# Kernel optimization log

Measured on AMD Instinct MI355X. Metric: run time of the kernel, lower is better.

The kernel has to match this reference:

```python
import jax, jax.numpy as jnp
import numpy as np

# Matcher weights (Deformable-DETR defaults used by SimPLR-style repos)
COST_CLASS, COST_BBOX, COST_GIOU = 2.0, 5.0, 2.0
ALPHA, GAMMA = 0.25, 2.0  # focal cost hyperparams
EPS = 1e-8


def box_cxcywh_to_xyxy(b):
    cx, cy, w, h = jnp.split(b, 4, axis=-1)
    return jnp.concatenate([cx - 0.5 * w, cy - 0.5 * h, cx + 0.5 * w, cy + 0.5 * h], axis=-1)


def generalized_box_iou(b1, b2):
    # b1 [Q,4], b2 [T,4] in xyxy -> [Q,T]
    area1 = (b1[:, 2] - b1[:, 0]) * (b1[:, 3] - b1[:, 1])
    area2 = (b2[:, 2] - b2[:, 0]) * (b2[:, 3] - b2[:, 1])
    lt = jnp.maximum(b1[:, None, :2], b2[None, :, :2])
    rb = jnp.minimum(b1[:, None, 2:], b2[None, :, 2:])
    wh = jnp.clip(rb - lt, 0.0)
    inter = wh[..., 0] * wh[..., 1]
    union = area1[:, None] + area2[None, :] - inter
    iou = inter / union
    lt2 = jnp.minimum(b1[:, None, :2], b2[None, :, :2])
    rb2 = jnp.maximum(b1[:, None, 2:], b2[None, :, 2:])
    wh2 = jnp.clip(rb2 - lt2, 0.0)
    hull = wh2[..., 0] * wh2[..., 1]
    return iou - (hull - union) / hull


def cost_matrix(logits, boxes, tgt_ids, tgt_boxes):
    # per-image: logits [Q,C], boxes [Q,4] cxcywh, tgt_ids [T], tgt_boxes [T,4]
    prob = jax.nn.sigmoid(logits)
    neg = (1.0 - ALPHA) * (prob ** GAMMA) * (-jnp.log(1.0 - prob + EPS))
    pos = ALPHA * ((1.0 - prob) ** GAMMA) * (-jnp.log(prob + EPS))
    cost_class = pos[:, tgt_ids] - neg[:, tgt_ids]                    # [Q,T]
    cost_bbox = jnp.abs(boxes[:, None, :] - tgt_boxes[None, :, :]).sum(-1)  # L1 cdist [Q,T]
    cost_giou = -generalized_box_iou(box_cxcywh_to_xyxy(boxes), box_cxcywh_to_xyxy(tgt_boxes))
    return COST_BBOX * cost_bbox + COST_CLASS * cost_class + COST_GIOU * cost_giou


def lsa(cost):
    # Hungarian (Jonker-Volgenant / e-maxx shortest augmenting path), minimizes.
    # cost [n, m] with n <= m; returns col4row: column assigned to each row.
    n, m = cost.shape
    u = np.zeros(n + 1)
    v = np.zeros(m + 1)
    p = np.zeros(m + 1, dtype=np.int64)   # p[j] = row matched to col j (1-based), 0 = free
    way = np.zeros(m + 1, dtype=np.int64)
    for i in range(1, n + 1):
        p[0] = i
        j0 = 0
        minv = np.full(m + 1, np.inf)
        used = np.zeros(m + 1, dtype=bool)
        while True:
            used[j0] = True
            i0 = p[j0]
            free = ~used
            free[0] = False
            cur = cost[i0 - 1] - u[i0] - v[1:]
            better = np.zeros(m + 1, dtype=bool)
            better[1:] = free[1:] & (cur < minv[1:])
            minv[better] = cur[better[1:]]
            way[better] = j0
            cand = np.where(free[1:], minv[1:], np.inf)
            j1 = int(np.argmin(cand)) + 1
            delta = cand[j1 - 1]
            u[p[used]] += delta
            v[used] -= delta
            minv[free] -= delta
            j0 = j1
            if p[j0] == 0:
                break
        while j0 != 0:
            j1 = way[j0]
            p[j0] = p[j1]
            j0 = j1
    col4row = np.zeros(n, dtype=np.int64)
    for j in range(1, m + 1):
        if p[j] > 0:
            col4row[p[j] - 1] = j - 1
    return col4row


_batched_cost = jax.jit(jax.vmap(cost_matrix, in_axes=(0, 0, 0, 0)))


def setup_inputs() -> dict:
    key = jax.random.key(0)
    k1, k2, k3, k4 = jax.random.split(key, 4)
    bs, nq, nc, nt = 32, 900, 1203, 100
    return {
        "pred_logits": jax.random.normal(k1, (bs, nq, nc), dtype=jnp.float32),
        "pred_boxes": jax.random.uniform(k2, (bs, nq, 4), dtype=jnp.float32),
        "tgt_labels": jax.random.randint(k3, (bs, nt), 0, nc, dtype=jnp.int64),
        "tgt_boxes": jax.random.uniform(k4, (bs, nt, 4), dtype=jnp.float32),
    }


def reference(pred_logits, pred_boxes, tgt_labels, tgt_boxes):
    # Cost blocks [bs, Q, T] (identical to the per-image diagonal blocks of the
    # torch code's [bs, Q, sum_T] view, which are the only parts used).
    C = _batched_cost(pred_logits, pred_boxes, tgt_labels, tgt_boxes)
    Cn = np.asarray(jax.device_get(C))
    rows, cols = [], []
    for b in range(Cn.shape[0]):
        col4row = lsa(Cn[b].T)          # [T]: matched query index per target
        order = np.argsort(col4row)     # scipy returns row indices sorted ascending
        rows.append(col4row[order])     # index_i: selected prediction indices
        cols.append(order)              # index_j: corresponding target indices
    pred_idx = jnp.asarray(np.stack(rows), dtype=jnp.int64)  # [bs, T]
    tgt_idx = jnp.asarray(np.stack(cols), dtype=jnp.int64)   # [bs, T]
    return C, pred_idx, tgt_idx
```

## Files before the change

kernel.cpp:

```cpp
#include <hip/hip_runtime.h>
#include <math.h>

#define BS 32
#define NQ 900
#define NC 1203
#define NT 100
#define SLOTS 15
#define K8 8

__device__ float g_CT[(size_t)BS * NT * NQ];
__device__ unsigned long long g_topk[(size_t)BS * NT * K8];

__device__ __forceinline__ unsigned long long packf(float f, int col) {
    unsigned k = __float_as_uint(f);
    k = (k & 0x80000000u) ? ~k : (k | 0x80000000u);
    return ((unsigned long long)k << 32) | (unsigned)col;
}
__device__ __forceinline__ float unpack_val(unsigned long long p) {
    unsigned k = (unsigned)(p >> 32);
    unsigned bits = (k & 0x80000000u) ? (k ^ 0x80000000u) : ~k;
    return __uint_as_float(bits);
}
__device__ __forceinline__ int unpack_col(unsigned long long p) {
    return (int)(p & 0xFFFFFFFFu);
}

__global__ __launch_bounds__(128) void cost_kernel(
    const float* __restrict__ logits, const float* __restrict__ boxes,
    const int* __restrict__ tlabels, const float* __restrict__ tboxes,
    float* __restrict__ C)
{
    int bq = blockIdx.x;
    int b = bq / NQ, q = bq % NQ;
    int t = threadIdx.x;

    const float* pb = boxes + (size_t)(b * NQ + q) * 4;
    float pcx = pb[0], pcy = pb[1], pw = pb[2], ph = pb[3];

    if (t < NT) {
        int id = tlabels[b * NT + t];
        float x = logits[(size_t)(b * NQ + q) * NC + id];
        float prob = 1.0f / (1.0f + expf(-x));
        float neg = 0.75f * (prob * prob) * (-logf(1.0f - prob + 1e-8f));
        float pos = 0.25f * ((1.0f - prob) * (1.0f - prob)) * (-logf(prob + 1e-8f));
        float cclass = pos - neg;

        const float* tb = tboxes + (size_t)(b * NT + t) * 4;
        float tcx = tb[0], tcy = tb[1], tw = tb[2], th = tb[3];
        float cbbox = fabsf(pcx - tcx) + fabsf(pcy - tcy) + fabsf(pw - tw) + fabsf(ph - th);

        float p0 = pcx - 0.5f * pw, p1 = pcy - 0.5f * ph;
        float p2 = pcx + 0.5f * pw, p3 = pcy + 0.5f * ph;
        float t0 = tcx - 0.5f * tw, t1 = tcy - 0.5f * th;
        float t2 = tcx + 0.5f * tw, t3 = tcy + 0.5f * th;
        float area1 = (p2 - p0) * (p3 - p1);
        float area2 = (t2 - t0) * (t3 - t1);
        float ltx = fmaxf(p0, t0), lty = fmaxf(p1, t1);
        float rbx = fminf(p2, t2), rby = fminf(p3, t3);
        float wx = fmaxf(rbx - ltx, 0.0f), wy = fmaxf(rby - lty, 0.0f);
        float inter = wx * wy;
        float uni = area1 + area2 - inter;
        float iou = inter / uni;
        float l2x = fminf(p0, t0), l2y = fminf(p1, t1);
        float r2x = fmaxf(p2, t2), r2y = fmaxf(p3, t3);
        float hx = fmaxf(r2x - l2x, 0.0f), hy = fmaxf(r2y - l2y, 0.0f);
        float hull = hx * hy;
        float giou = iou - (hull - uni) / hull;

        C[(size_t)(b * NQ + q) * NT + t] =
            5.0f * cbbox + 2.0f * cclass + 2.0f * (-giou);
    }
}

__global__ __launch_bounds__(256) void transpose_kernel(const float* __restrict__ C)
{
    __shared__ float tile[64][101];
    int b = blockIdx.x / 15;
    int chunk = blockIdx.x % 15;
    int q0 = chunk * 64;
    int nq = (q0 + 64 <= NQ) ? 64 : (NQ - q0);
    int tid = threadIdx.x;

    const float* Cb = C + (size_t)b * NQ * NT;
    for (int e = tid; e < nq * NT; e += 256) {
        int qq = e / NT, t = e % NT;
        tile[qq][t] = Cb[(size_t)(q0 + qq) * NT + t];
    }
    __syncthreads();
    float* CTb = g_CT + (size_t)b * NT * NQ;
    for (int e = tid; e < NT * nq; e += 256) {
        int t = e / nq, qq = e % nq;
        CTb[(size_t)t * NQ + q0 + qq] = tile[qq][t];
    }
}

__global__ __launch_bounds__(64) void topk_kernel()
{
    int bi = blockIdx.x;
    const float* row = g_CT + (size_t)bi * NQ;
    int lane = threadIdx.x;

    unsigned long long r[K8];
    #pragma unroll
    for (int m = 0; m < K8; ++m) r[m] = 0xFFFFFFFFFFFFFFFFull;

    #pragma unroll
    for (int k = 0; k < SLOTS; ++k) {
        int j = (k << 6) + lane;
        if ((k < SLOTS - 1) || (j < NQ)) {
            unsigned long long key = packf(row[j], j);
            #pragma unroll
            for (int m = 0; m < K8; ++m) {
                unsigned long long lo = key < r[m] ? key : r[m];
                unsigned long long hi = key < r[m] ? r[m] : key;
                r[m] = lo; key = hi;
            }
        }
    }
    #pragma unroll
    for (int off = 32; off; off >>= 1) {
        unsigned long long bv[K8], t[K8];
        #pragma unroll
        for (int m = 0; m < K8; ++m) bv[m] = __shfl_down(r[m], off);
        #pragma unroll
        for (int m = 0; m < K8; ++m) {
            unsigned long long x = bv[K8 - 1 - m];
            t[m] = r[m] < x ? r[m] : x;
        }
        #pragma unroll
        for (int d = 4; d; d >>= 1) {
            #pragma unroll
            for (int m = 0; m < K8; ++m) {
                if (!(m & d)) {
                    unsigned long long a = t[m], b2 = t[m | d];
                    t[m] = a < b2 ? a : b2;
                    t[m | d] = a < b2 ? b2 : a;
                }
            }
        }
        #pragma unroll
        for (int m = 0; m < K8; ++m) r[m] = t[m];
    }
    if (lane == 0) {
        #pragma unroll
        for (int m = 0; m < K8; ++m) g_topk[(size_t)bi * K8 + m] = r[m];
    }
}

__global__ __launch_bounds__(64) void jv_kernel(
    float* __restrict__ pred_out, float* __restrict__ tgt_out)
{
    int b = blockIdx.x;
    const float* CTb = g_CT + (size_t)b * NT * NQ;
    int lane = threadIdx.x;
    const double INF = __builtin_huge_val();

    __shared__ double u[NT];
    __shared__ double vsh[NQ];
    __shared__ double distA[128];
    __shared__ int pathA[128];
    __shared__ int asgCols[128];
    __shared__ int pos4col[NQ];
    __shared__ int row4col[NQ];
    __shared__ int col4row[NT];
    __shared__ int aminsh[NT];
    __shared__ int freeRows[NT + 4];
    __shared__ int parked[NT];
    __shared__ int srList[140];
    __shared__ unsigned long long tksh[NT][K8];
    __shared__ unsigned char visits[NT];
    __shared__ int nFreeSh, nParkSh, asgCountSh;

    for (int j = lane; j < NQ; j += 64) { vsh[j] = 0.0; row4col[j] = 0x7fffffff; pos4col[j] = -1; }
    {
        const unsigned long long* src = g_topk + (size_t)b * NT * K8;
        for (int e = lane; e < NT * K8; e += 64) ((unsigned long long*)tksh)[e] = src[e];
    }
    for (int i = lane; i < NT; i += 64) { col4row[i] = -1; visits[i] = 0; }
    if (lane == 0) { nFreeSh = 0; nParkSh = 0; asgCountSh = 0; }
    __syncthreads();
    for (int i = lane; i < NT; i += 64) {
        unsigned long long tk = tksh[i][0];
        aminsh[i] = unpack_col(tk);
        u[i] = (double)unpack_val(tk);
    }
    __syncthreads();

    for (int i = lane; i < NT; i += 64) atomicMin(&row4col[aminsh[i]], i);
    __syncthreads();
    if (lane == 0) {
        int n = 0, cnt = 0;
        for (int i = 0; i < NT; ++i) {
            int j = aminsh[i];
            if (row4col[j] == i) { col4row[i] = j; pos4col[j] = cnt; asgCols[cnt++] = j; }
            else freeRows[n++] = i;
        }
        nFreeSh = n; asgCountSh = cnt;
    }
    __syncthreads();
    for (int j = lane; j < NQ; j += 64)
        if (row4col[j] == 0x7fffffff) row4col[j] = -1;
    __syncthreads();

    int guard = 0;
    while (guard++ < 300) {
        int nf = nFreeSh;
        if (nf == 0) break;
        int i = freeRows[nf - 1];
        if (visits[i] >= 2) {
            if (lane == 0) { nFreeSh = nf - 1; parked[nParkSh] = i; nParkSh++; }
            __syncthreads();
            continue;
        }
        if (lane == 0) visits[i]++;
        int asgCount = asgCountSh;
        const float* rowp = CTb + (size_t)i * NQ;

        double m1 = INF, m2 = INF; int j1 = -1;
        bool haveFree = (lane < K8) && (row4col[unpack_col(tksh[i][lane])] < 0);
        unsigned long long bal = __ballot(haveFree);
        if (__popcll(bal) >= 2) {
            #pragma unroll
            for (int s = 0; s < 2; ++s) {
                int pos = lane + (s << 6);
                if (pos < asgCount) {
                    int j = asgCols[pos];
                    double cur = (double)rowp[j] - vsh[j];
                    if (cur < m1) { m2 = m1; m1 = cur; j1 = j; }
                    else if (cur < m2) m2 = cur;
                }
            }
            if (haveFree) {
                unsigned long long tk = tksh[i][lane];
                double cur = (double)unpack_val(tk);
                int j = unpack_col(tk);
                if (cur < m1) { m2 = m1; m1 = cur; j1 = j; }
                else if (cur < m2) m2 = cur;
            }
        } else {
            #pragma unroll
            for (int k = 0; k < SLOTS; ++k) {
                int j = (k << 6) + lane;
                if ((k < SLOTS - 1) || (j < NQ)) {
                    double cur = (double)rowp[j] - vsh[j];
                    if (cur < m1) { m2 = m1; m1 = cur; j1 = j; }
                    else if (cur < m2) m2 = cur;
                }
            }
        }
        for (int off = 32; off; off >>= 1) {
            double o1 = __shfl_down(m1, off); int oj = __shfl_down(j1, off);
            double o2 = __shfl_down(m2, off);
            if (o1 < m1 || (o1 == m1 && (unsigned)oj < (unsigned)j1)) { m2 = fmin(m1, o2); m1 = o1; j1 = oj; }
            else m2 = fmin(m2, o1);
        }
        if (lane == 0) {
            u[i] = m2;
            vsh[j1] -= (m2 - m1);
            int inc = row4col[j1];
            row4col[j1] = i; col4row[i] = j1;
            int n = nf - 1;
            if (inc >= 0) { col4row[inc] = -1; freeRows[n++] = inc; }
            else { pos4col[j1] = asgCountSh; asgCols[asgCountSh] = j1; asgCountSh++; }
            nFreeSh = n;
        }
        __syncthreads();
    }
    if (lane == 0) {
        while (nFreeSh > 0) { nFreeSh--; parked[nParkSh] = freeRows[nFreeSh]; nParkSh++; }
    }
    __syncthreads();

    int np = nParkSh;
    for (int f = 0; f < np; ++f) {
        int curRow = parked[f];
        int asgCount = asgCountSh;
        double mvA = INF, mvB = INF;
        bool pA = false, pB = false;
        for (int pos = lane; pos < asgCount; pos += 64) distA[pos] = INF;
        double bestFree = INF; int bfCol = -1, bfRow = -1;
        double minVal = 0.0; int i = curRow; int nSr = 1;
        if (lane == 0) srList[0] = curRow;
        __syncthreads();

        int g2 = 0; bool sink = false;
        while (!sink && g2++ < 120) {
            const float* rowp = CTb + (size_t)i * NQ;
            double ui = u[i];
            {
                int pos = lane;
                if (pos < asgCount && !pA) {
                    int j = asgCols[pos];
                    double cur = minVal + (double)rowp[j] - ui - vsh[j];
                    if (cur < mvA) { mvA = cur; distA[pos] = cur; pathA[pos] = i; }
                }
                pos = lane + 64;
                if (pos < asgCount && !pB) {
                    int j = asgCols[pos];
                    double cur = minVal + (double)rowp[j] - ui - vsh[j];
                    if (cur < mvB) { mvB = cur; distA[pos] = cur; pathA[pos] = i; }
                }
            }
            double fc = INF; int fj = -1;
            if (lane < K8) {
                unsigned long long tk = tksh[i][lane];
                int j = unpack_col(tk);
                if (row4col[j] < 0) { fc = minVal + (double)unpack_val(tk) - ui; fj = j; }
            }
            if (__ballot(fc < INF) == 0ull) {
                #pragma unroll
                for (int k = 0; k < SLOTS; ++k) {
                    int j = (k << 6) + lane;
                    if (((k < SLOTS - 1) || (j < NQ)) && row4col[j] < 0) {
                        double cur = minVal + (double)rowp[j] - ui;
                        if (cur < fc) { fc = cur; fj = j; }
                    }
                }
            }
            double pv; int ppos;
            double pva = pA ? INF : mvA, pvb = pB ? INF : mvB;
            if (pvb < pva) { pv = pvb; ppos = lane + 64; } else { pv = pva; ppos = lane; }
            for (int off = 32; off; off >>= 1) {
                double o = __shfl_down(pv, off); int op = __shfl_down(ppos, off);
                if (o < pv || (o == pv && op < ppos)) { pv = o; ppos = op; }
                double of = __shfl_down(fc, off); int ofj = __shfl_down(fj, off);
                if (of < fc || (of == fc && (unsigned)ofj < (unsigned)fj)) { fc = of; fj = ofj; }
            }
            pv = __shfl(pv, 0); ppos = __shfl(ppos, 0);
            fc = __shfl(fc, 0); fj = __shfl(fj, 0);
            if (fc < bestFree) { bestFree = fc; bfCol = fj; bfRow = i; }
            if (bestFree <= pv) { minVal = bestFree; sink = true; }
            else {
                minVal = pv;
                if (lane == (ppos & 63)) { if (ppos < 64) pA = true; else pB = true; }
                i = row4col[asgCols[ppos]];
                if (lane == 0) srList[nSr] = i;
                nSr++;
            }
        }
        __syncthreads();

        if (lane == 0) {
            u[curRow] += minVal;
            for (int t2 = 1; t2 < nSr; ++t2) {
                int ri = srList[t2];
                u[ri] += minVal - distA[pos4col[col4row[ri]]];
            }
        }
        {
            int pos = lane;
            if (pos < asgCount && pA) vsh[asgCols[pos]] -= minVal - distA[pos];
            pos = lane + 64;
            if (pos < asgCount && pB) vsh[asgCols[pos]] -= minVal - distA[pos];
        }
        if (lane == 0) {
            int j = bfCol, ri = bfRow; int g3 = 0;
            while (g3++ < 128) {
                row4col[j] = ri;
                int tj = col4row[ri]; col4row[ri] = j;
                if (ri == curRow) break;
                j = tj; ri = pathA[pos4col[j]];
            }
            pos4col[bfCol] = asgCountSh; asgCols[asgCountSh] = bfCol; asgCountSh++;
        }
        __syncthreads();
    }

    for (int i2 = lane; i2 < NT; i2 += 64) {
        int ci = col4row[i2];
        int rank = 0;
        for (int k2 = 0; k2 < NT; ++k2) rank += (col4row[k2] < ci);
        pred_out[b * NT + rank] = (float)ci;
        tgt_out[b * NT + rank] = (float)i2;
    }
}

extern "C" void kernel_launch(void* const* d_in, const int* in_sizes, int n_in,
                              void* d_out, int out_size, void* d_ws, size_t ws_size,
                              hipStream_t stream) {
    const float* logits = (const float*)d_in[0];
    const float* boxes  = (const float*)d_in[1];
    const int*   tlab   = (const int*)d_in[2];
    const float* tboxes = (const float*)d_in[3];

    float* out  = (float*)d_out;
    float* C    = out;
    float* pred = out + (size_t)BS * NQ * NT;
    float* tgt  = pred + BS * NT;

    cost_kernel<<<BS * NQ, 128, 0, stream>>>(logits, boxes, tlab, tboxes, C);
    transpose_kernel<<<BS * 15, 256, 0, stream>>>(C);
    topk_kernel<<<BS * NT, 64, 0, stream>>>();
    jv_kernel<<<BS, 64, 0, stream>>>(pred, tgt);
}
```

Before: 109.0 us.

## Fuse transpose and top-k selection into one kernel over target-row chunks

Merges the transpose kernel and the per-row top-k kernel into a single kernel. Each block loads 8 target columns for all queries into shared memory, writes the transposed rows to the global buffer, and runs the top-8 selection directly from shared memory, one wavefront per row. This removes a kernel launch and the re-read of the transposed matrix from global memory. In exchange there are far fewer blocks (416), and the strided loads of 8 floats per query row may coalesce poorly.

```diff
diff --git a/kernel.cpp b/kernel.cpp
--- a/kernel.cpp
+++ b/kernel.cpp
@@ -7,6 +7,8 @@
 #define NT 100
 #define SLOTS 15
 #define K8 8
+#define TCH 8
+#define NCHUNK 13
 
 __device__ float g_CT[(size_t)BS * NT * NQ];
 __device__ unsigned long long g_topk[(size_t)BS * NT * K8];
@@ -72,78 +74,78 @@
     }
 }
 
-__global__ __launch_bounds__(256) void transpose_kernel(const float* __restrict__ C)
+__global__ __launch_bounds__(256) void ttopk_kernel(const float* __restrict__ C)
 {
-    __shared__ float tile[64][101];
-    int b = blockIdx.x / 15;
-    int chunk = blockIdx.x % 15;
-    int q0 = chunk * 64;
-    int nq = (q0 + 64 <= NQ) ? 64 : (NQ - q0);
+    __shared__ float tile[TCH][NQ];
+    int blk = blockIdx.x;
+    int b = blk / NCHUNK, chunk = blk % NCHUNK;
+    int t0 = chunk * TCH;
+    int nrows = (t0 + TCH <= NT) ? TCH : (NT - t0);
     int tid = threadIdx.x;
+    int w = tid >> 6, lane = tid & 63;
 
     const float* Cb = C + (size_t)b * NQ * NT;
-    for (int e = tid; e < nq * NT; e += 256) {
-        int qq = e / NT, t = e % NT;
-        tile[qq][t] = Cb[(size_t)(q0 + qq) * NT + t];
-    }
-    __syncthreads();
+    for (int e = tid; e < NQ * TCH; e += 256) {
+        int q = e >> 3, tt = e & 7;
+        if (tt < nrows) tile[tt][q] = Cb[(size_t)q * NT + t0 + tt];
+    }
+    __syncthreads();
+
     float* CTb = g_CT + (size_t)b * NT * NQ;
-    for (int e = tid; e < NT * nq; e += 256) {
-        int t = e / nq, qq = e % nq;
-        CTb[(size_t)t * NQ + q0 + qq] = tile[qq][t];
-    }
-}
-
-__global__ __launch_bounds__(64) void topk_kernel()
-{
-    int bi = blockIdx.x;
-    const float* row = g_CT + (size_t)bi * NQ;
-    int lane = threadIdx.x;
-
-    unsigned long long r[K8];
-    #pragma unroll
-    for (int m = 0; m < K8; ++m) r[m] = 0xFFFFFFFFFFFFFFFFull;
-
-    #pragma unroll
-    for (int k = 0; k < SLOTS; ++k) {
-        int j = (k << 6) + lane;
-        if ((k < SLOTS - 1) || (j < NQ)) {
-            unsigned long long key = packf(row[j], j);
+    for (int tt = 0; tt < nrows; ++tt)
+        for (int q = tid; q < NQ; q += 256)
+            CTb[(size_t)(t0 + tt) * NQ + q] = tile[tt][q];
+
+    for (int pass = 0; pass < 2; ++pass) {
+        int tt = w + pass * 4;
+        if (tt >= nrows) continue;
+
+        unsigned long long r[K8];
+        #pragma unroll
+        for (int m = 0; m < K8; ++m) r[m] = 0xFFFFFFFFFFFFFFFFull;
+
+        #pragma unroll
+        for (int k = 0; k < SLOTS; ++k) {
+            int j = (k << 6) + lane;
+            if ((k < SLOTS - 1) || (j < NQ)) {
+                unsigned long long key = packf(tile[tt][j], j);
+                #pragma unroll
+                for (int m = 0; m < K8; ++m) {
+                    unsigned long long lo = key < r[m] ? key : r[m];
+                    unsigned long long hi = key < r[m] ? r[m] : key;
+                    r[m] = lo; key = hi;
+                }
+            }
+        }
+        #pragma unroll
+        for (int off = 32; off; off >>= 1) {
+            unsigned long long bv[K8], tmp[K8];
+            #pragma unroll
+            for (int m = 0; m < K8; ++m) bv[m] = __shfl_down(r[m], off);
             #pragma unroll
             for (int m = 0; m < K8; ++m) {
-                unsigned long long lo = key < r[m] ? key : r[m];
-                unsigned long long hi = key < r[m] ? r[m] : key;
-                r[m] = lo; key = hi;
-            }
-        }
-    }
-    #pragma unroll
-    for (int off = 32; off; off >>= 1) {
-        unsigned long long bv[K8], t[K8];
-        #pragma unroll
-        for (int m = 0; m < K8; ++m) bv[m] = __shfl_down(r[m], off);
-        #pragma unroll
-        for (int m = 0; m < K8; ++m) {
-            unsigned long long x = bv[K8 - 1 - m];
-            t[m] = r[m] < x ? r[m] : x;
-        }
-        #pragma unroll
-        for (int d = 4; d; d >>= 1) {
-            #pragma unroll
-            for (int m = 0; m < K8; ++m) {
-                if (!(m & d)) {
-                    unsigned long long a = t[m], b2 = t[m | d];
-                    t[m] = a < b2 ? a : b2;
-                    t[m | d] = a < b2 ? b2 : a;
-                }
-            }
-        }
-        #pragma unroll
-        for (int m = 0; m < K8; ++m) r[m] = t[m];
-    }
-    if (lane == 0) {
-        #pragma unroll
-        for (int m = 0; m < K8; ++m) g_topk[(size_t)bi * K8 + m] = r[m];
+                unsigned long long x = bv[K8 - 1 - m];
+                tmp[m] = r[m] < x ? r[m] : x;
+            }
+            #pragma unroll
+            for (int d = 4; d; d >>= 1) {
+                #pragma unroll
+                for (int m = 0; m < K8; ++m) {
+                    if (!(m & d)) {
+                        unsigned long long a = tmp[m], b2 = tmp[m | d];
+                        tmp[m] = a < b2 ? a : b2;
+                        tmp[m | d] = a < b2 ? b2 : a;
+                    }
+                }
+            }
+            #pragma unroll
+            for (int m = 0; m < K8; ++m) r[m] = tmp[m];
+        }
+        if (lane == 0) {
+            #pragma unroll
+            for (int m = 0; m < K8; ++m)
+                g_topk[(size_t)(b * NT + t0 + tt) * K8 + m] = r[m];
+        }
     }
 }
 
@@ -389,7 +391,6 @@
     float* tgt  = pred + BS * NT;
 
     cost_kernel<<<BS * NQ, 128, 0, stream>>>(logits, boxes, tlab, tboxes, C);
-    transpose_kernel<<<BS * 15, 256, 0, stream>>>(C);
-    topk_kernel<<<BS * NT, 64, 0, stream>>>();
+    ttopk_kernel<<<BS * NCHUNK, 256, 0, stream>>>(C);
     jv_kernel<<<BS, 64, 0, stream>>>(pred, tgt);
 }
```

Measured after the change: 128.8 us. 18.1% more time.

## Run JV auction phase with four wavefronts bidding on free rows concurrently

Applied to the files above, without the earlier changes.

The JV kernel grows from one wavefront to four. In the auction phase each wavefront computes the bid for a different free row, and thread 0 then applies the bids serially, requeueing any row whose bid clashes with an earlier one. The kernel also reads the untransposed C output with a strided access of stride NT instead of the transposed g_CT rows, which makes the row scans uncoalesced. The augmenting-path phase still runs on wave 0 alone, with extra shared-memory handoffs and barriers. The change may also alter the auction's visit order and so the final assignment.

```diff
diff --git a/kernel.cpp b/kernel.cpp
--- a/kernel.cpp
+++ b/kernel.cpp
@@ -7,6 +7,8 @@
 #define NT 100
 #define SLOTS 15
 #define K8 8
+#define JBLK 256
+#define NW 4
 
 __device__ float g_CT[(size_t)BS * NT * NQ];
 __device__ unsigned long long g_topk[(size_t)BS * NT * K8];
@@ -119,27 +121,27 @@
     }
     #pragma unroll
     for (int off = 32; off; off >>= 1) {
-        unsigned long long bv[K8], t[K8];
+        unsigned long long bv[K8], tmp[K8];
         #pragma unroll
         for (int m = 0; m < K8; ++m) bv[m] = __shfl_down(r[m], off);
         #pragma unroll
         for (int m = 0; m < K8; ++m) {
             unsigned long long x = bv[K8 - 1 - m];
-            t[m] = r[m] < x ? r[m] : x;
+            tmp[m] = r[m] < x ? r[m] : x;
         }
         #pragma unroll
         for (int d = 4; d; d >>= 1) {
             #pragma unroll
             for (int m = 0; m < K8; ++m) {
                 if (!(m & d)) {
-                    unsigned long long a = t[m], b2 = t[m | d];
-                    t[m] = a < b2 ? a : b2;
-                    t[m | d] = a < b2 ? b2 : a;
+                    unsigned long long a = tmp[m], b2 = tmp[m | d];
+                    tmp[m] = a < b2 ? a : b2;
+                    tmp[m | d] = a < b2 ? b2 : a;
                 }
             }
         }
         #pragma unroll
-        for (int m = 0; m < K8; ++m) r[m] = t[m];
+        for (int m = 0; m < K8; ++m) r[m] = tmp[m];
     }
     if (lane == 0) {
         #pragma unroll
@@ -147,12 +149,14 @@
     }
 }
 
-__global__ __launch_bounds__(64) void jv_kernel(
+__global__ __launch_bounds__(JBLK) void jv_kernel(
+    const float* __restrict__ C,
     float* __restrict__ pred_out, float* __restrict__ tgt_out)
 {
     int b = blockIdx.x;
-    const float* CTb = g_CT + (size_t)b * NT * NQ;
-    int lane = threadIdx.x;
+    const float* Cb = C + (size_t)b * NQ * NT;
+    int tid = threadIdx.x;
+    int w = tid >> 6, lane = tid & 63;
     const double INF = __builtin_huge_val();
 
     __shared__ double u[NT];
@@ -164,31 +168,33 @@
     __shared__ int row4col[NQ];
     __shared__ int col4row[NT];
     __shared__ int aminsh[NT];
-    __shared__ int freeRows[NT + 4];
+    __shared__ int freeRows[NT + 8];
     __shared__ int parked[NT];
     __shared__ int srList[140];
     __shared__ unsigned long long tksh[NT][K8];
     __shared__ unsigned char visits[NT];
+    __shared__ double pm1[NW], pm2[NW];
+    __shared__ int pj1[NW], prow[NW];
     __shared__ int nFreeSh, nParkSh, asgCountSh;
 
-    for (int j = lane; j < NQ; j += 64) { vsh[j] = 0.0; row4col[j] = 0x7fffffff; pos4col[j] = -1; }
+    for (int j = tid; j < NQ; j += JBLK) { vsh[j] = 0.0; row4col[j] = 0x7fffffff; pos4col[j] = -1; }
     {
         const unsigned long long* src = g_topk + (size_t)b * NT * K8;
-        for (int e = lane; e < NT * K8; e += 64) ((unsigned long long*)tksh)[e] = src[e];
-    }
-    for (int i = lane; i < NT; i += 64) { col4row[i] = -1; visits[i] = 0; }
-    if (lane == 0) { nFreeSh = 0; nParkSh = 0; asgCountSh = 0; }
-    __syncthreads();
-    for (int i = lane; i < NT; i += 64) {
+        for (int e = tid; e < NT * K8; e += JBLK) ((unsigned long long*)tksh)[e] = src[e];
+    }
+    for (int i = tid; i < NT; i += JBLK) { col4row[i] = -1; visits[i] = 0; }
+    if (tid == 0) { nFreeSh = 0; nParkSh = 0; asgCountSh = 0; }
+    __syncthreads();
+    for (int i = tid; i < NT; i += JBLK) {
         unsigned long long tk = tksh[i][0];
         aminsh[i] = unpack_col(tk);
         u[i] = (double)unpack_val(tk);
     }
     __syncthreads();
 
-    for (int i = lane; i < NT; i += 64) atomicMin(&row4col[aminsh[i]], i);
-    __syncthreads();
-    if (lane == 0) {
+    for (int i = tid; i < NT; i += JBLK) atomicMin(&row4col[aminsh[i]], i);
+    __syncthreads();
+    if (tid == 0) {
         int n = 0, cnt = 0;
         for (int i = 0; i < NT; ++i) {
             int j = aminsh[i];
@@ -198,75 +204,85 @@
         nFreeSh = n; asgCountSh = cnt;
     }
     __syncthreads();
-    for (int j = lane; j < NQ; j += 64)
+    for (int j = tid; j < NQ; j += JBLK)
         if (row4col[j] == 0x7fffffff) row4col[j] = -1;
     __syncthreads();
 
     int guard = 0;
-    while (guard++ < 300) {
+    while (guard++ < 250) {
         int nf = nFreeSh;
         if (nf == 0) break;
-        int i = freeRows[nf - 1];
-        if (visits[i] >= 2) {
-            if (lane == 0) { nFreeSh = nf - 1; parked[nParkSh] = i; nParkSh++; }
-            __syncthreads();
-            continue;
-        }
-        if (lane == 0) visits[i]++;
-        int asgCount = asgCountSh;
-        const float* rowp = CTb + (size_t)i * NQ;
-
-        double m1 = INF, m2 = INF; int j1 = -1;
-        bool haveFree = (lane < K8) && (row4col[unpack_col(tksh[i][lane])] < 0);
-        unsigned long long bal = __ballot(haveFree);
-        if (__popcll(bal) >= 2) {
-            #pragma unroll
-            for (int s = 0; s < 2; ++s) {
-                int pos = lane + (s << 6);
-                if (pos < asgCount) {
-                    int j = asgCols[pos];
-                    double cur = (double)rowp[j] - vsh[j];
+        int take = nf < NW ? nf : NW;
+        if (w < take) {
+            int i = freeRows[nf - 1 - w];
+            int asgCount = asgCountSh;
+
+            double m1 = INF, m2 = INF; int j1 = -1;
+            bool haveFree = (lane < K8) && (row4col[unpack_col(tksh[i][lane])] < 0);
+            unsigned long long bal = __ballot(haveFree);
+            if (__popcll(bal) >= 2) {
+                #pragma unroll
+                for (int s = 0; s < 2; ++s) {
+                    int pos = lane + (s << 6);
+                    if (pos < asgCount) {
+                        int j = asgCols[pos];
+                        double cur = (double)Cb[(size_t)j * NT + i] - vsh[j];
+                        if (cur < m1) { m2 = m1; m1 = cur; j1 = j; }
+                        else if (cur < m2) m2 = cur;
+                    }
+                }
+                if (haveFree) {
+                    unsigned long long tk = tksh[i][lane];
+                    double cur = (double)unpack_val(tk);
+                    int j = unpack_col(tk);
                     if (cur < m1) { m2 = m1; m1 = cur; j1 = j; }
                     else if (cur < m2) m2 = cur;
                 }
-            }
-            if (haveFree) {
-                unsigned long long tk = tksh[i][lane];
-                double cur = (double)unpack_val(tk);
-                int j = unpack_col(tk);
-                if (cur < m1) { m2 = m1; m1 = cur; j1 = j; }
-                else if (cur < m2) m2 = cur;
-            }
-        } else {
-            #pragma unroll
-            for (int k = 0; k < SLOTS; ++k) {
-                int j = (k << 6) + lane;
-                if ((k < SLOTS - 1) || (j < NQ)) {
-                    double cur = (double)rowp[j] - vsh[j];
-                    if (cur < m1) { m2 = m1; m1 = cur; j1 = j; }
-                    else if (cur < m2) m2 = cur;
-                }
-            }
-        }
-        for (int off = 32; off; off >>= 1) {
-            double o1 = __shfl_down(m1, off); int oj = __shfl_down(j1, off);
-            double o2 = __shfl_down(m2, off);
-            if (o1 < m1 || (o1 == m1 && (unsigned)oj < (unsigned)j1)) { m2 = fmin(m1, o2); m1 = o1; j1 = oj; }
-            else m2 = fmin(m2, o1);
-        }
-        if (lane == 0) {
-            u[i] = m2;
-            vsh[j1] -= (m2 - m1);
-            int inc = row4col[j1];
-            row4col[j1] = i; col4row[i] = j1;
-            int n = nf - 1;
-            if (inc >= 0) { col4row[inc] = -1; freeRows[n++] = inc; }
-            else { pos4col[j1] = asgCountSh; asgCols[asgCountSh] = j1; asgCountSh++; }
+            } else {
+                #pragma unroll
+                for (int k = 0; k < SLOTS; ++k) {
+                    int j = (k << 6) + lane;
+                    if ((k < SLOTS - 1) || (j < NQ)) {
+                        double cur = (double)Cb[(size_t)j * NT + i] - vsh[j];
+                        if (cur < m1) { m2 = m1; m1 = cur; j1 = j; }
+                        else if (cur < m2) m2 = cur;
+                    }
+                }
+            }
+            for (int off = 32; off; off >>= 1) {
+                double o1 = __shfl_down(m1, off); int oj = __shfl_down(j1, off);
+                double o2 = __shfl_down(m2, off);
+                if (o1 < m1 || (o1 == m1 && (unsigned)oj < (unsigned)j1)) { m2 = fmin(m1, o2); m1 = o1; j1 = oj; }
+                else m2 = fmin(m2, o1);
+            }
+            if (lane == 0) { pm1[w] = m1; pm2[w] = m2; pj1[w] = j1; prow[w] = i; }
+        }
+        __syncthreads();
+        if (tid == 0) {
+            int n = nf - take;
+            int cj[NW]; int nc = 0;
+            for (int k = 0; k < take; ++k) {
+                int i = prow[k];
+                if (visits[i] >= 2) { parked[nParkSh] = i; nParkSh++; continue; }
+                int j1 = pj1[k];
+                bool clash = false;
+                for (int k2 = 0; k2 < nc; ++k2) if (cj[k2] == j1) clash = true;
+                if (clash) { freeRows[n++] = i; continue; }
+                cj[nc++] = j1;
+                visits[i]++;
+                double m1 = pm1[k], m2 = pm2[k];
+                u[i] = m2;
+                vsh[j1] -= (m2 - m1);
+                int inc = row4col[j1];
+                row4col[j1] = i; col4row[i] = j1;
+                if (inc >= 0) { col4row[inc] = -1; freeRows[n++] = inc; }
+                else { pos4col[j1] = asgCountSh; asgCols[asgCountSh] = j1; asgCountSh++; }
+            }
             nFreeSh = n;
         }
         __syncthreads();
     }
-    if (lane == 0) {
+    if (tid == 0) {
         while (nFreeSh > 0) { nFreeSh--; parked[nParkSh] = freeRows[nFreeSh]; nParkSh++; }
     }
     __syncthreads();
@@ -277,96 +293,102 @@
         int asgCount = asgCountSh;
         double mvA = INF, mvB = INF;
         bool pA = false, pB = false;
-        for (int pos = lane; pos < asgCount; pos += 64) distA[pos] = INF;
         double bestFree = INF; int bfCol = -1, bfRow = -1;
         double minVal = 0.0; int i = curRow; int nSr = 1;
-        if (lane == 0) srList[0] = curRow;
+        if (w == 0) {
+            for (int pos = lane; pos < asgCount; pos += 64) distA[pos] = INF;
+            if (lane == 0) srList[0] = curRow;
+        }
         __syncthreads();
 
-        int g2 = 0; bool sink = false;
-        while (!sink && g2++ < 120) {
-            const float* rowp = CTb + (size_t)i * NQ;
-            double ui = u[i];
-            {
-                int pos = lane;
-                if (pos < asgCount && !pA) {
-                    int j = asgCols[pos];
-                    double cur = minVal + (double)rowp[j] - ui - vsh[j];
-                    if (cur < mvA) { mvA = cur; distA[pos] = cur; pathA[pos] = i; }
-                }
-                pos = lane + 64;
-                if (pos < asgCount && !pB) {
-                    int j = asgCols[pos];
-                    double cur = minVal + (double)rowp[j] - ui - vsh[j];
-                    if (cur < mvB) { mvB = cur; distA[pos] = cur; pathA[pos] = i; }
-                }
-            }
-            double fc = INF; int fj = -1;
-            if (lane < K8) {
-                unsigned long long tk = tksh[i][lane];
-                int j = unpack_col(tk);
-                if (row4col[j] < 0) { fc = minVal + (double)unpack_val(tk) - ui; fj = j; }
-            }
-            if (__ballot(fc < INF) == 0ull) {
-                #pragma unroll
-                for (int k = 0; k < SLOTS; ++k) {
-                    int j = (k << 6) + lane;
-                    if (((k < SLOTS - 1) || (j < NQ)) && row4col[j] < 0) {
-                        double cur = minVal + (double)rowp[j] - ui;
-                        if (cur < fc) { fc = cur; fj = j; }
+        if (w == 0) {
+            int g2 = 0; bool sink = false;
+            while (!sink && g2++ < 120) {
+                double ui = u[i];
+                {
+                    int pos = lane;
+                    if (pos < asgCount && !pA) {
+                        int j = asgCols[pos];
+                        double cur = minVal + (double)Cb[(size_t)j * NT + i] - ui - vsh[j];
+                        if (cur < mvA) { mvA = cur; distA[pos] = cur; pathA[pos] = i; }
                     }
-                }
-            }
-            double pv; int ppos;
-            double pva = pA ? INF : mvA, pvb = pB ? INF : mvB;
-            if (pvb < pva) { pv = pvb; ppos = lane + 64; } else { pv = pva; ppos = lane; }
-            for (int off = 32; off; off >>= 1) {
-                double o = __shfl_down(pv, off); int op = __shfl_down(ppos, off);
-                if (o < pv || (o == pv && op < ppos)) { pv = o; ppos = op; }
-                double of = __shfl_down(fc, off); int ofj = __shfl_down(fj, off);
-                if (of < fc || (of == fc && (unsigned)ofj < (unsigned)fj)) { fc = of; fj = ofj; }
-            }
-            pv = __shfl(pv, 0); ppos = __shfl(ppos, 0);
-            fc = __shfl(fc, 0); fj = __shfl(fj, 0);
-            if (fc < bestFree) { bestFree = fc; bfCol = fj; bfRow = i; }
-            if (bestFree <= pv) { minVal = bestFree; sink = true; }
-            else {
-                minVal = pv;
-                if (lane == (ppos & 63)) { if (ppos < 64) pA = true; else pB = true; }
-                i = row4col[asgCols[ppos]];
-                if (lane == 0) srList[nSr] = i;
-                nSr++;
-            }
+                    pos = lane + 64;
+                    if (pos < asgCount && !pB) {
+                        int j = asgCols[pos];
+                        double cur = minVal + (double)Cb[(size_t)j * NT + i] - ui - vsh[j];
+                        if (cur < mvB) { mvB = cur; distA[pos] = cur; pathA[pos] = i; }
+                    }
+                }
+                double fc = INF; int fj = -1;
+                if (lane < K8) {
+                    unsigned long long tk = tksh[i][lane];
+                    int j = unpack_col(tk);
+                    if (row4col[j] < 0) { fc = minVal + (double)unpack_val(tk) - ui; fj = j; }
+                }
+                if (__ballot(fc < INF) == 0ull) {
+                    #pragma unroll
+                    for (int k = 0; k < SLOTS; ++k) {
+                        int j = (k << 6) + lane;
+                        if (((k < SLOTS - 1) || (j < NQ)) && row4col[j] < 0) {
+                            double cur = minVal + (double)Cb[(size_t)j * NT + i] - ui;
+                            if (cur < fc) { fc = cur; fj = j; }
+                        }
+                    }
+                }
+                double pv; int ppos;
+                double pva = pA ? INF : mvA, pvb = pB ? INF : mvB;
+                if (pvb < pva) { pv = pvb; ppos = lane + 64; } else { pv = pva; ppos = lane; }
+                for (int off = 32; off; off >>= 1) {
+                    double o = __shfl_down(pv, off); int op = __shfl_down(ppos, off);
+                    if (o < pv || (o == pv && op < ppos)) { pv = o; ppos = op; }
+                    double of = __shfl_down(fc, off); int ofj = __shfl_down(fj, off);
+                    if (of < fc || (of == fc && (unsigned)ofj < (unsigned)fj)) { fc = of; fj = ofj; }
+                }
+                pv = __shfl(pv, 0); ppos = __shfl(ppos, 0);
+                fc = __shfl(fc, 0); fj = __shfl(fj, 0);
+                if (fc < bestFree) { bestFree = fc; bfCol = fj; bfRow = i; }
+                if (bestFree <= pv) { minVal = bestFree; sink = true; }
+                else {
+                    minVal = pv;
+                    if (lane == (ppos & 63)) { if (ppos < 64) pA = true; else pB = true; }
+                    i = row4col[asgCols[ppos]];
+                    if (lane == 0) srList[nSr] = i;
+                    nSr++;
+                }
+            }
+            if (lane == 0) { pm1[0] = minVal; pj1[0] = bfCol; prow[0] = bfRow; pm2[0] = (double)nSr; }
         }
         __syncthreads();
 
-        if (lane == 0) {
-            u[curRow] += minVal;
-            for (int t2 = 1; t2 < nSr; ++t2) {
+        if (tid == 0) {
+            double mv = pm1[0]; int ns = (int)pm2[0];
+            u[curRow] += mv;
+            for (int t2 = 1; t2 < ns; ++t2) {
                 int ri = srList[t2];
-                u[ri] += minVal - distA[pos4col[col4row[ri]]];
-            }
-        }
-        {
+                u[ri] += mv - distA[pos4col[col4row[ri]]];
+            }
+        }
+        if (w == 0) {
+            double mv = pm1[0];
             int pos = lane;
-            if (pos < asgCount && pA) vsh[asgCols[pos]] -= minVal - distA[pos];
+            if (pos < asgCount && pA) vsh[asgCols[pos]] -= mv - distA[pos];
             pos = lane + 64;
-            if (pos < asgCount && pB) vsh[asgCols[pos]] -= minVal - distA[pos];
-        }
-        if (lane == 0) {
-            int j = bfCol, ri = bfRow; int g3 = 0;
+            if (pos < asgCount && pB) vsh[asgCols[pos]] -= mv - distA[pos];
+        }
+        if (tid == 0) {
+            int j = pj1[0], ri = prow[0]; int g3 = 0;
             while (g3++ < 128) {
                 row4col[j] = ri;
                 int tj = col4row[ri]; col4row[ri] = j;
                 if (ri == curRow) break;
                 j = tj; ri = pathA[pos4col[j]];
             }
-            pos4col[bfCol] = asgCountSh; asgCols[asgCountSh] = bfCol; asgCountSh++;
+            pos4col[pj1[0]] = asgCountSh; asgCols[asgCountSh] = pj1[0]; asgCountSh++;
         }
         __syncthreads();
     }
 
-    for (int i2 = lane; i2 < NT; i2 += 64) {
+    for (int i2 = tid; i2 < NT; i2 += JBLK) {
         int ci = col4row[i2];
         int rank = 0;
         for (int k2 = 0; k2 < NT; ++k2) rank += (col4row[k2] < ci);
@@ -391,5 +413,5 @@
     cost_kernel<<<BS * NQ, 128, 0, stream>>>(logits, boxes, tlab, tboxes, C);
     transpose_kernel<<<BS * 15, 256, 0, stream>>>(C);
     topk_kernel<<<BS * NT, 64, 0, stream>>>();
-    jv_kernel<<<BS, 64, 0, stream>>>(pred, tgt);
-}
+    jv_kernel<<<BS, JBLK, 0, stream>>>(C, pred, tgt);
+}
```

New measurement: 91.56 us. 1.19x faster.
